# Performance work log

Hardware: AMD Instinct MI355X
Metric: run time of the kernel (lower is better)

## Reference

```python
import jax, jax.numpy as jnp
import numpy as np

KERNEL_SIZE = 3


def extract_local_features(feature_map, point_coords, kernel_size=KERNEL_SIZE):
    # feature_map: (B,C,H,W); point_coords: (B,N,2) normalized (y,x) in [0,1]
    B, C, H, W = feature_map.shape
    half = kernel_size // 2
    x = (point_coords[..., 1] * (W - 1)).astype(jnp.int32)  # (B,N)
    y = (point_coords[..., 0] * (H - 1)).astype(jnp.int32)
    x_min = jnp.clip(x - half, 0, None)
    x_max = jnp.clip(x + half + 1, None, W)
    y_min = jnp.clip(y - half, 0, None)
    y_max = jnpp_clip = jnp.clip(y + half + 1, None, H)
    y_max = jnp.clip(y + half + 1, None, H)
    # gather a fixed (k,k) window with clamped offsets, mask out-of-window entries
    offs = jnp.arange(kernel_size)  # (k,)
    yy = y_min[..., None] + offs  # (B,N,k) candidate rows
    xx = x_min[..., None] + offs  # (B,N,k)
    y_valid = yy < y_max[..., None]
    x_valid = xx < x_max[..., None]
    yy_c = jnp.clip(yy, 0, H - 1)
    xx_c = jnp.clip(xx, 0, W - 1)
    # flat spatial indices (B,N,k,k)
    flat_idx = yy_c[..., :, None] * W + xx_c[..., None, :]
    valid = (y_valid[..., :, None] & x_valid[..., None, :]).astype(feature_map.dtype)
    fm_flat = feature_map.reshape(B, C, H * W)  # (B,C,HW)

    def per_batch(fm, idx, val):
        # fm: (C,HW); idx,val: (N,k,k)
        g = fm[:, idx.reshape(-1)].reshape(fm.shape[0], *idx.shape)  # (C,N,k,k)
        s = jnp.einsum('cnij,nij->cn', g, val)
        cnt = val.sum(axis=(-1, -2))  # (N,)
        return s / cnt[None, :]

    return jax.vmap(per_batch)(fm_flat, flat_idx, valid)  # (B,C,N)


def point_sample(inp, point_coords):
    # bilinear grid_sample, align_corners=False, coords in [0,1] as (x,y) order
    # per the code: grid = 2*coords - 1; grid_sample uses (x,y) convention
    B, C, H, W = inp.shape
    gx = point_coords[..., 0]  # (B,N) in [0,1]
    gy = point_coords[..., 1]
    # align_corners=False mapping: pix = ((g*2-1)+1)/2 * size - 0.5 = g*size - 0.5
    fx = gx * W - 0.5
    fy = gy * H - 0.5
    x0 = jnp.floor(fx).astype(jnp.int32)
    y0 = jnp.floor(fy).astype(jnp.int32)
    wx = fx - x0
    wy = fy - y0

    def gather(yc, xc):
        inb = ((yc >= 0) & (yc < H) & (xc >= 0) & (xc < W)).astype(inp.dtype)  # (B,N)
        ycc = jnp.clip(yc, 0, H - 1)
        xcc = jnp.clip(xc, 0, W - 1)
        flat = ycc * W + xcc  # (B,N)
        fm = inp.reshape(B, C, H * W)
        g = jax.vmap(lambda f, i: f[:, i])(fm, flat)  # (B,C,N)
        return g * inb[:, None, :]

    v00 = gather(y0, x0)
    v01 = gather(y0, x0 + 1)
    v10 = gather(y0 + 1, x0)
    v11 = gather(y0 + 1, x0 + 1)
    wx_ = wx[:, None, :]
    wy_ = wy[:, None, :]
    out = (v00 * (1 - wx_) * (1 - wy_) + v01 * wx_ * (1 - wy_)
           + v10 * (1 - wx_) * wy_ + v11 * wx_ * wy_)  # (B,C,N)
    return out.transpose(0, 2, 1)  # (B,N,C)


def calculate_uncertainty(mask_logits):
    return -jnp.abs(mask_logits).squeeze(1)  # (B,H,W)


def edge_topk_sampling(edge_masks, uncertainty_map, topk):
    # edge_masks: (B,H,W) {0,1}; uncertainty_map: (B,H,W)
    B, H, W = edge_masks.shape
    NEG = jnp.asarray(-1e30, uncertainty_map.dtype)
    masked_u = jnp.where(edge_masks.reshape(B, -1) == 1,
                         uncertainty_map.reshape(B, -1), NEG)
    vals, idx = jax.lax.top_k(masked_u, topk)  # (B,topk)
    yi = (idx // W).astype(jnp.float32)
    xi = (idx % W).astype(jnp.float32)
    coords = jnp.stack([yi / (H - 1), xi / (W - 1)], axis=-1)  # (B,topk,2) (y,x)
    return idx, coords


def setup_inputs() -> dict:
    key = jax.random.key(0)
    k1, k2, k3, k4 = jax.random.split(key, 4)
    B, C, H, W = 8, 256, 256, 256
    N = 4096
    feature_map = jax.random.normal(k1, (B, C, H, W), dtype=jnp.float32)
    pred_mask = jax.random.normal(k2, (B, 1, H, W), dtype=jnp.float32)
    edge_masks = jax.random.randint(k3, (B, H, W), 0, 2).astype(jnp.int32)
    point_coords = jax.random.uniform(k4, (B, N, 2), dtype=jnp.float32)
    return {"feature_map": feature_map, "pred_mask": pred_mask,
            "edge_masks": edge_masks, "point_coords": point_coords,
            "topk": 4096}


def reference(feature_map, pred_mask, edge_masks, point_coords, topk):
    uncertainty_map = calculate_uncertainty(pred_mask)  # (B,H,W)
    idx, important_coords = edge_topk_sampling(edge_masks, uncertainty_map, topk)
    local_feats = extract_local_features(feature_map, important_coords)  # (B,C,topk)
    sampled = point_sample(feature_map, point_coords)  # (B,N,C)
    return local_feats, sampled, important_coords, idx
```

## Files before the change

kernel.cpp:

```cpp
#include <hip/hip_runtime.h>

#define CC 256
#define HH 256
#define WW 256
#define HWV 65536
#define NN 4096
#define SROWS 18
#define SSTRIDE 260

using u64 = unsigned long long;
using u32 = unsigned int;

__device__ __forceinline__ u32 lbound(const u32* __restrict__ a, u32 n, u32 key) {
    u32 lo = 0, hi = n;
    while (lo < hi) { u32 mid = (lo + hi) >> 1; if (a[mid] < key) lo = mid + 1; else hi = mid; }
    return lo;
}

__global__ void build_keys_k(const float* __restrict__ pm, const int* __restrict__ em,
                             u64* __restrict__ keys) {
    int i = blockIdx.x * blockDim.x + threadIdx.x;
    float f = (em[i] == 1) ? -fabsf(pm[i]) : -1e30f;
    u32 u = __float_as_uint(f);
    u32 k = (u & 0x80000000u) ? ~u : (u | 0x80000000u);
    u32 pix = (u32)i & 0xFFFFu;
    keys[i] = ((u64)k << 16) | (u64)(0xFFFFu - pix);
}

template<int DIRECT>
__global__ __launch_bounds__(1024) void topk_sortpc_k(const u64* __restrict__ keys,
                                                      const float* __restrict__ pc,
                                                      u32* __restrict__ stash,
                                                      u32* __restrict__ pixSorted,
                                                      u32* __restrict__ pcSorted,
                                                      float* __restrict__ outCoord,
                                                      float* __restrict__ outIdx) {
    __shared__ u64 sel[NN];
    __shared__ u64 bm[1024];
    __shared__ u32 wp[1024];
    __shared__ u32 s_digit, s_rem, s_cnt;
    const int t = threadIdx.x;
    if (blockIdx.x < 8) {
        const int b = blockIdx.x;
        const u64* kb = keys + (size_t)b * HWV;
        u32* hist = (u32*)sel;
        u64 prefix = 0ULL;
        u32 remaining = NN;
        for (int r = 0; r < 4; ++r) {
            int shift = 36 - 12 * r;
            #pragma unroll
            for (int q = 0; q < 4; ++q) hist[t + q * 1024] = 0u;
            __syncthreads();
            for (int i = t; i < HWV; i += 1024) {
                u64 K = kb[i];
                if ((K >> (shift + 12)) == prefix)
                    atomicAdd(&hist[(u32)((K >> shift) & 0xFFFULL)], 1u);
            }
            __syncthreads();
            for (int off = 1; off < 4096; off <<= 1) {
                u32 v[4];
                #pragma unroll
                for (int q = 0; q < 4; ++q) {
                    int i = t + q * 1024;
                    v[q] = hist[i];
                    if (i + off < 4096) v[q] += hist[i + off];
                }
                __syncthreads();
                #pragma unroll
                for (int q = 0; q < 4; ++q) hist[t + q * 1024] = v[q];
                __syncthreads();
            }
            #pragma unroll
            for (int q = 0; q < 4; ++q) {
                int d = t + q * 1024;
                u32 ge = hist[d];
                u32 gt = (d < 4095) ? hist[d + 1] : 0u;
                if (ge >= remaining && gt < remaining) { s_digit = (u32)d; s_rem = remaining - gt; }
            }
            __syncthreads();
            prefix = (prefix << 12) | (u64)s_digit;
            remaining = s_rem;
            __syncthreads();
        }
        if (t == 0) s_cnt = 0u;
        __syncthreads();
        for (int i = t; i < HWV; i += 1024) {
            u64 K = kb[i];
            if (K >= prefix) { u32 p = atomicAdd(&s_cnt, 1u); sel[p] = K; }
        }
        __syncthreads();
        for (int k = 2; k <= NN; k <<= 1) {
            for (int j = k >> 1; j > 0; j >>= 1) {
                for (int i = t; i < NN; i += 1024) {
                    int l = i ^ j;
                    if (l > i) {
                        u64 a = sel[i], c = sel[l];
                        bool asc = ((i & k) == 0);
                        if ((a < c) == asc) { sel[i] = c; sel[l] = a; }
                    }
                }
                __syncthreads();
            }
        }
        bm[t] = 0ULL;
        __syncthreads();
        #pragma unroll
        for (int q = 0; q < 4; ++q) {
            int r = t + q * 1024;
            u32 pix = 0xFFFFu - (u32)(sel[r] & 0xFFFFULL);
            if (DIRECT) {
                u32 yi = pix >> 8, xi = pix & 255u;
                outCoord[((size_t)b * NN + r) * 2 + 0] = (float)yi / 255.0f;
                outCoord[((size_t)b * NN + r) * 2 + 1] = (float)xi / 255.0f;
                outIdx[b * NN + r] = (float)pix;
            } else {
                stash[b * NN + r] = pix;
            }
            atomicOr(&bm[pix >> 6], 1ULL << (pix & 63));
        }
        __syncthreads();
        wp[t] = (u32)__popcll(bm[t]);
        __syncthreads();
        for (int off = 1; off < 1024; off <<= 1) {
            u32 v = wp[t];
            if (t >= off) v += wp[t - off];
            __syncthreads();
            wp[t] = v;
            __syncthreads();
        }
        #pragma unroll
        for (int q = 0; q < 4; ++q) {
            int r = t + q * 1024;
            u32 pix = 0xFFFFu - (u32)(sel[r] & 0xFFFFULL);
            int w = (int)(pix >> 6);
            u32 pos = wp[w] - (u32)__popcll(bm[w])
                    + (u32)__popcll(bm[w] & ((1ULL << (pix & 63)) - 1ULL));
            pixSorted[b * NN + pos] = (pix << 12) | (u32)r;
        }
    } else {
        const int b = blockIdx.x - 8;
        u32* cellArr = (u32*)sel;
        u32* hist256 = wp;
        u32* cnt     = (u32*)bm;
        if (t < 256) { hist256[t] = 0u; cnt[t] = 0u; }
        __syncthreads();
        for (int n = t; n < NN; n += 1024) {
            float gx = pc[((size_t)b * NN + n) * 2 + 0];
            float gy = pc[((size_t)b * NN + n) * 2 + 1];
            float fx = gx * 256.0f - 0.5f;
            float fy = gy * 256.0f - 0.5f;
            int x0 = (int)floorf(fx), y0 = (int)floorf(fy);
            int xc = min(max(x0, 0), 255), yc = min(max(y0, 0), 255);
            cellArr[n] = ((u32)(yc * 256 + xc) << 12) | (u32)n;
            atomicAdd(&hist256[yc], 1u);
        }
        __syncthreads();
        for (int off = 1; off < 256; off <<= 1) {
            u32 v = 0;
            if (t < 256) { v = hist256[t]; if (t >= off) v += hist256[t - off]; }
            __syncthreads();
            if (t < 256) hist256[t] = v;
            __syncthreads();
        }
        for (int n = t; n < NN; n += 1024) {
            u32 pk = cellArr[n];
            u32 yc = pk >> 20;
            u32 base = (yc > 0) ? hist256[yc - 1] : 0u;
            u32 pos = base + atomicAdd(&cnt[yc], 1u);
            pcSorted[b * NN + pos] = pk;
        }
    }
}

#define STAGE_LOAD(plane) \
    { int idx, r, c4, gr; \
      idx = t;        r = idx >> 6; c4 = idx & 63; gr = min(max(rStart + r, 0), HH - 1); \
      g0 = *(const float4*)((plane) + gr * WW + c4 * 4); \
      idx = t + 256;  r = idx >> 6; c4 = idx & 63; gr = min(max(rStart + r, 0), HH - 1); \
      g1 = *(const float4*)((plane) + gr * WW + c4 * 4); \
      idx = t + 512;  r = idx >> 6; c4 = idx & 63; gr = min(max(rStart + r, 0), HH - 1); \
      g2 = *(const float4*)((plane) + gr * WW + c4 * 4); \
      idx = t + 768;  r = idx >> 6; c4 = idx & 63; gr = min(max(rStart + r, 0), HH - 1); \
      g3 = *(const float4*)((plane) + gr * WW + c4 * 4); \
      if (t < 128) { idx = t + 1024; r = idx >> 6; c4 = idx & 63; gr = min(max(rStart + r, 0), HH - 1); \
      g4 = *(const float4*)((plane) + gr * WW + c4 * 4); } }

#define STAGE_WRITE() \
    { int idx, r, c4; \
      idx = t;        r = idx >> 6; c4 = idx & 63; *(float4*)(sm + r * SSTRIDE + c4 * 4) = g0; \
      idx = t + 256;  r = idx >> 6; c4 = idx & 63; *(float4*)(sm + r * SSTRIDE + c4 * 4) = g1; \
      idx = t + 512;  r = idx >> 6; c4 = idx & 63; *(float4*)(sm + r * SSTRIDE + c4 * 4) = g2; \
      idx = t + 768;  r = idx >> 6; c4 = idx & 63; *(float4*)(sm + r * SSTRIDE + c4 * 4) = g3; \
      if (t < 128) { idx = t + 1024; r = idx >> 6; c4 = idx & 63; *(float4*)(sm + r * SSTRIDE + c4 * 4) = g4; } }

__global__ __launch_bounds__(256) void plane_gather_k(const float* __restrict__ fm,
                                                      const float* __restrict__ pc,
                                                      const u32* __restrict__ pixSorted,
                                                      const u32* __restrict__ pcSorted,
                                                      float* __restrict__ outLc,
                                                      float* __restrict__ outSc) {
    __shared__ float sm[SROWS * SSTRIDE];
    const int band = blockIdx.x, c0 = blockIdx.y * 32, b = blockIdx.z;
    const int t = threadIdx.x;
    const int rStart = band * 16 - 1;
    const u32 keyLo = (u32)band << 24, keyHi = (u32)(band + 1) << 24;
    const u32* aL = pixSorted + b * NN;
    const u32* aS = pcSorted + b * NN;
    u32 loL = lbound(aL, NN, keyLo), cL = lbound(aL, NN, keyHi) - loL;
    u32 loS = lbound(aS, NN, keyLo), cS = lbound(aS, NN, keyHi) - loS;
    const float* planes = fm + ((size_t)b * CC + c0) * HWV;
    const float* pcb = pc + (size_t)b * NN * 2;

    int  Lo0 = 0, Lc2 = 0, Lr2 = 0;   float Lwc = 0, Lwr = 0, Lic = 0;
    int  Mo0 = 0, Mc2 = 0, Mr2 = 0;   float Mwc = 0, Mwr = 0, Mic = 0;
    int  So0 = 0, Sr1 = 0;            float Sv0 = 0, Sv1 = 0, Sw0 = 0, Sw1 = 0;
    int  To0 = 0, Tr1 = 0;            float Tv0 = 0, Tv1 = 0, Tw0 = 0, Tw1 = 0;
    {
        u32 jl = (u32)t;
        if (jl < cL) {
            u32 pix = aL[loL + jl] >> 12;
            int yi = (int)(pix >> 8), xi = (int)(pix & 255u);
            float cy = (float)yi / 255.0f, cx = (float)xi / 255.0f;
            int x = (int)(cx * 255.0f), y = (int)(cy * 255.0f);
            int x_min = max(x - 1, 0), wid = min(x + 2, WW) - x_min;
            int y_min = max(y - 1, 0), hgt = min(y + 2, HH) - y_min;
            Lo0 = (y_min - rStart) * SSTRIDE + x_min;
            Lc2 = (wid == 3) ? 2 : 0;  Lwc = (wid == 3) ? 1.0f : 0.0f;
            Lr2 = ((hgt == 3) ? 2 : 0) * SSTRIDE;  Lwr = (hgt == 3) ? 1.0f : 0.0f;
            Lic = 1.0f / (float)(wid * hgt);
        }
        jl = 256u + (u32)t;
        if (jl < cL) {
            u32 pix = aL[loL + jl] >> 12;
            int yi = (int)(pix >> 8), xi = (int)(pix & 255u);
            float cy = (float)yi / 255.0f, cx = (float)xi / 255.0f;
            int x = (int)(cx * 255.0f), y = (int)(cy * 255.0f);
            int x_min = max(x - 1, 0), wid = min(x + 2, WW) - x_min;
            int y_min = max(y - 1, 0), hgt = min(y + 2, HH) - y_min;
            Mo0 = (y_min - rStart) * SSTRIDE + x_min;
            Mc2 = (wid == 3) ? 2 : 0;  Mwc = (wid == 3) ? 1.0f : 0.0f;
            Mr2 = ((hgt == 3) ? 2 : 0) * SSTRIDE;  Mwr = (hgt == 3) ? 1.0f : 0.0f;
            Mic = 1.0f / (float)(wid * hgt);
        }
        u32 js = (u32)t;
        if (js < cS) {
            u32 sn = aS[loS + js] & 0xFFFu;
            float gx = pcb[2 * sn + 0], gy = pcb[2 * sn + 1];
            float fx = gx * 256.0f - 0.5f, fy = gy * 256.0f - 0.5f;
            float fx0 = floorf(fx), fy0 = floorf(fy);
            int x0 = (int)fx0, y0 = (int)fy0;
            float wx = fx - fx0, wy = fy - fy0;
            int xb = min(max(x0, 0), WW - 2);
            if (x0 < 0)            { Sv0 = wx;        Sv1 = 0.0f; }
            else if (x0 >= WW - 1) { Sv0 = 0.0f;      Sv1 = 1.0f - wx; }
            else                   { Sv0 = 1.0f - wx; Sv1 = wx; }
            Sw0 = (y0 >= 0)     ? (1.0f - wy) : 0.0f;
            Sw1 = (y0 + 1 < HH) ? wy          : 0.0f;
            int yc0 = min(max(y0, 0), HH - 1), yc1 = min(max(y0 + 1, 0), HH - 1);
            So0 = (yc0 - rStart) * SSTRIDE + xb;
            Sr1 = (yc1 - yc0) * SSTRIDE;
        }
        js = 256u + (u32)t;
        if (js < cS) {
            u32 sn = aS[loS + js] & 0xFFFu;
            float gx = pcb[2 * sn + 0], gy = pcb[2 * sn + 1];
            float fx = gx * 256.0f - 0.5f, fy = gy * 256.0f - 0.5f;
            float fx0 = floorf(fx), fy0 = floorf(fy);
            int x0 = (int)fx0, y0 = (int)fy0;
            float wx = fx - fx0, wy = fy - fy0;
            int xb = min(max(x0, 0), WW - 2);
            if (x0 < 0)            { Tv0 = wx;        Tv1 = 0.0f; }
            else if (x0 >= WW - 1) { Tv0 = 0.0f;      Tv1 = 1.0f - wx; }
            else                   { Tv0 = 1.0f - wx; Tv1 = wx; }
            Tw0 = (y0 >= 0)     ? (1.0f - wy) : 0.0f;
            Tw1 = (y0 + 1 < HH) ? wy          : 0.0f;
            int yc0 = min(max(y0, 0), HH - 1), yc1 = min(max(y0 + 1, 0), HH - 1);
            To0 = (yc0 - rStart) * SSTRIDE + xb;
            Tr1 = (yc1 - yc0) * SSTRIDE;
        }
    }

    float4 g0, g1, g2, g3, g4;
    STAGE_LOAD(planes)
    STAGE_WRITE()
    __syncthreads();

    #pragma unroll 1
    for (int j = 0; j < 32; ++j) {
        if (j + 1 < 32) { const float* np = planes + (size_t)(j + 1) * HWV; STAGE_LOAD(np) }
        float* oL = outLc + ((size_t)(b * CC + c0 + j)) * NN + loL;
        float* oS = outSc + ((size_t)(b * CC + c0 + j)) * NN + loS;
        if ((u32)t < cL) {
            float r0 = sm[Lo0] + sm[Lo0 + 1] + Lwc * sm[Lo0 + Lc2];
            float r1 = sm[Lo0 + SSTRIDE] + sm[Lo0 + SSTRIDE + 1] + Lwc * sm[Lo0 + SSTRIDE + Lc2];
            int o2 = Lo0 + Lr2;
            float r2 = sm[o2] + sm[o2 + 1] + Lwc * sm[o2 + Lc2];
            oL[t] = (r0 + r1 + Lwr * r2) * Lic;
        }
        if (256u + (u32)t < cL) {
            float r0 = sm[Mo0] + sm[Mo0 + 1] + Mwc * sm[Mo0 + Mc2];
            float r1 = sm[Mo0 + SSTRIDE] + sm[Mo0 + SSTRIDE + 1] + Mwc * sm[Mo0 + SSTRIDE + Mc2];
            int o2 = Mo0 + Mr2;
            float r2 = sm[o2] + sm[o2 + 1] + Mwc * sm[o2 + Mc2];
            oL[256 + t] = (r0 + r1 + Mwr * r2) * Mic;
        }
        if ((u32)t < cS) {
            oS[t] = Sw0 * (sm[So0] * Sv0 + sm[So0 + 1] * Sv1)
                  + Sw1 * (sm[So0 + Sr1] * Sv0 + sm[So0 + Sr1 + 1] * Sv1);
        }
        if (256u + (u32)t < cS) {
            oS[256 + t] = Tw0 * (sm[To0] * Tv0 + sm[To0 + 1] * Tv1)
                        + Tw1 * (sm[To0 + Tr1] * Tv0 + sm[To0 + Tr1 + 1] * Tv1);
        }
        __syncthreads();
        if (j + 1 < 32) { STAGE_WRITE() }
        __syncthreads();
    }

    for (u32 jl = 512 + (u32)t; jl < cL; jl += 256) {
        u32 pix = aL[loL + jl] >> 12;
        int yi = (int)(pix >> 8), xi = (int)(pix & 255u);
        float cy = (float)yi / 255.0f, cx = (float)xi / 255.0f;
        int x = (int)(cx * 255.0f), y = (int)(cy * 255.0f);
        int x_min = max(x - 1, 0), x_max = min(x + 2, WW);
        int y_min = max(y - 1, 0), y_max = min(y + 2, HH);
        float ic = 1.0f / (float)((x_max - x_min) * (y_max - y_min));
        for (int j = 0; j < 32; ++j) {
            const float* p = planes + (size_t)j * HWV;
            float s = 0.0f;
            for (int yy = y_min; yy < y_max; ++yy)
                for (int xx = x_min; xx < x_max; ++xx) s += p[yy * WW + xx];
            outLc[((size_t)(b * CC + c0 + j)) * NN + loL + jl] = s * ic;
        }
    }
    for (u32 js = 512 + (u32)t; js < cS; js += 256) {
        u32 sn = aS[loS + js] & 0xFFFu;
        float gx = pcb[2 * sn + 0], gy = pcb[2 * sn + 1];
        float fx = gx * 256.0f - 0.5f, fy = gy * 256.0f - 0.5f;
        float fx0 = floorf(fx), fy0 = floorf(fy);
        int x0 = (int)fx0, y0 = (int)fy0;
        float wx = fx - fx0, wy = fy - fy0;
        int xb = min(max(x0, 0), WW - 2);
        float v0, v1, r0, r1;
        if (x0 < 0)            { v0 = wx;        v1 = 0.0f; }
        else if (x0 >= WW - 1) { v0 = 0.0f;      v1 = 1.0f - wx; }
        else                   { v0 = 1.0f - wx; v1 = wx; }
        r0 = (y0 >= 0)     ? (1.0f - wy) : 0.0f;
        r1 = (y0 + 1 < HH) ? wy          : 0.0f;
        int yc0 = min(max(y0, 0), HH - 1), yc1 = min(max(y0 + 1, 0), HH - 1);
        int o0 = yc0 * WW + xb, o1 = yc1 * WW + xb;
        for (int j = 0; j < 32; ++j) {
            const float* p = planes + (size_t)j * HWV;
            outSc[((size_t)(b * CC + c0 + j)) * NN + loS + js] =
                r0 * (p[o0] * v0 + p[o0 + 1] * v1) + r1 * (p[o1] * v0 + p[o1 + 1] * v1);
        }
    }
}

__global__ __launch_bounds__(256) void unpermL_k(const float* __restrict__ outLc,
                                                 const u32* __restrict__ pixSorted,
                                                 float* __restrict__ outL) {
    __shared__ float row[NN];
    const int c = blockIdx.x, b = blockIdx.y;
    const int t = threadIdx.x;
    const float* in = outLc + ((size_t)(b * CC + c)) * NN;
    for (int j = t; j < NN; j += 256)
        row[pixSorted[b * NN + j] & 0xFFFu] = in[j];
    __syncthreads();
    float* o = outL + ((size_t)(b * CC + c)) * NN;
    for (int i = t; i < NN; i += 256) o[i] = row[i];
}

__global__ __launch_bounds__(256) void unpermS_k(const float* __restrict__ outSc,
                                                 const u32* __restrict__ pcSorted,
                                                 float* __restrict__ outS) {
    __shared__ float tile[32][257];
    __shared__ u32 ns[256];
    const int j0 = blockIdx.x * 256, c0 = blockIdx.y * 32, b = blockIdx.z;
    const int t = threadIdx.x;
    ns[t] = pcSorted[b * NN + j0 + t] & 0xFFFu;
    for (int i = 0; i < 32; ++i)
        tile[i][t] = outSc[((size_t)(b * CC + c0 + i)) * NN + j0 + t];
    __syncthreads();
    for (int idx = t; idx < 8192; idx += 256) {
        int p = idx >> 5, k = idx & 31;
        outS[((size_t)b * NN + ns[p]) * CC + c0 + k] = tile[k][p];
    }
}

template<int MODE>
__global__ __launch_bounds__(256, 4) void gather_k(const float* __restrict__ fm,
                                                   const float* __restrict__ pc,
                                                   const u32* __restrict__ pixSorted,
                                                   const u32* __restrict__ pcSorted,
                                                   float* __restrict__ outLp,
                                                   float* __restrict__ outS) {
    __shared__ float tile[256][33];
    __shared__ u32 pidx[256];
    const int b = blockIdx.z, j0 = blockIdx.x * 256, t = threadIdx.x;
    bool doL; int c0;
    if (MODE == 1) { doL = true; c0 = blockIdx.y * 32; }
    else { doL = false; c0 = blockIdx.y * 32; }
    const float* planes = fm + ((size_t)b * CC + c0) * HWV;
    if (doL) {
        u32 packed = pixSorted[b * NN + j0 + t];
        u32 pix = packed >> 12;
        pidx[t] = packed & 0xFFFu;
        int yi = (int)(pix >> 8), xi = (int)(pix & 255u);
        float cy = (float)yi / 255.0f, cx = (float)xi / 255.0f;
        int x = (int)(cx * 255.0f), y = (int)(cy * 255.0f);
        int x_min = max(x - 1, 0), x_max = min(x + 2, WW);
        int y_min = max(y - 1, 0), y_max = min(y + 2, HH);
        int base = min(x_min & ~3, WW - 8);
        float w8[8];
        #pragma unroll
        for (int i = 0; i < 8; ++i)
            w8[i] = (base + i >= x_min && base + i < x_max) ? 1.0f : 0.0f;
        float wr2 = (y_min + 2 < y_max) ? 1.0f : 0.0f;
        int o0 = y_min * WW + base, o1 = o0 + WW;
        int o2 = min(y_min + 2, HH - 1) * WW + base;
        float invc = 1.0f / (float)((x_max - x_min) * (y_max - y_min));
        #pragma unroll 2
        for (int j = 0; j < 32; ++j) {
            const float* p = planes + (size_t)j * HWV;
            float4 a0 = *(const float4*)(p + o0), b0 = *(const float4*)(p + o0 + 4);
            float4 a1 = *(const float4*)(p + o1), b1 = *(const float4*)(p + o1 + 4);
            float4 a2 = *(const float4*)(p + o2), b2 = *(const float4*)(p + o2 + 4);
            float s0 = a0.x * w8[0] + a0.y * w8[1] + a0.z * w8[2] + a0.w * w8[3]
                     + b0.x * w8[4] + b0.y * w8[5] + b0.z * w8[6] + b0.w * w8[7];
            float s1 = a1.x * w8[0] + a1.y * w8[1] + a1.z * w8[2] + a1.w * w8[3]
                     + b1.x * w8[4] + b1.y * w8[5] + b1.z * w8[6] + b1.w * w8[7];
            float s2 = a2.x * w8[0] + a2.y * w8[1] + a2.z * w8[2] + a2.w * w8[3]
                     + b2.x * w8[4] + b2.y * w8[5] + b2.z * w8[6] + b2.w * w8[7];
            tile[t][j] = (s0 + s1 + wr2 * s2) * invc;
        }
        __syncthreads();
        for (int idx = t; idx < 8192; idx += 256) {
            int p = idx >> 5, k = idx & 31;
            outLp[((size_t)b * NN + pidx[p]) * CC + c0 + k] = tile[p][k];
        }
    } else {
        int n = (int)(pcSorted[b * NN + j0 + t] & 0xFFFu);
        pidx[t] = (u32)n;
        float gx = pc[((size_t)b * NN + n) * 2 + 0];
        float gy = pc[((size_t)b * NN + n) * 2 + 1];
        float fx = gx * 256.0f - 0.5f, fy = gy * 256.0f - 0.5f;
        float fx0 = floorf(fx), fy0 = floorf(fy);
        int x0 = (int)fx0, y0 = (int)fy0;
        float wx = fx - fx0, wy = fy - fy0;
        int xb = min(max(x0, 0), WW - 2);
        float wv0, wv1;
        if (x0 < 0)            { wv0 = wx;        wv1 = 0.0f; }
        else if (x0 >= WW - 1) { wv0 = 0.0f;      wv1 = 1.0f - wx; }
        else                   { wv0 = 1.0f - wx; wv1 = wx; }
        float wr0 = (y0 >= 0)     ? (1.0f - wy) : 0.0f;
        float wr1 = (y0 + 1 < HH) ? wy          : 0.0f;
        int yc0 = min(max(y0, 0), HH - 1), yc1 = min(max(y0 + 1, 0), HH - 1);
        int o0 = yc0 * WW + xb, o1 = yc1 * WW + xb;
        #pragma unroll 4
        for (int j = 0; j < 32; ++j) {
            const float* p = planes + (size_t)j * HWV;
            tile[t][j] = wr0 * (p[o0] * wv0 + p[o0 + 1] * wv1)
                       + wr1 * (p[o1] * wv0 + p[o1 + 1] * wv1);
        }
        __syncthreads();
        for (int idx = t; idx < 8192; idx += 256) {
            int p = idx >> 5, k = idx & 31;
            outS[((size_t)b * NN + pidx[p]) * CC + c0 + k] = tile[p][k];
        }
    }
}

__global__ __launch_bounds__(256) void transpose_k(const float* __restrict__ outLp,
                                                   float* __restrict__ outL) {
    __shared__ float tile[256][33];
    const int b = blockIdx.z, c0 = blockIdx.y * 32, r0 = blockIdx.x * 256;
    const int t = threadIdx.x;
    for (int idx = t; idx < 8192; idx += 256) {
        int p = idx >> 5, k = idx & 31;
        tile[p][k] = outLp[((size_t)b * NN + r0 + p) * CC + c0 + k];
    }
    __syncthreads();
    for (int idx = t; idx < 8192; idx += 256) {
        int cl = idx >> 8, col = idx & 255;
        outL[((size_t)b * CC + c0 + cl) * NN + r0 + col] = tile[col][cl];
    }
}

__global__ void emit_k(const u32* __restrict__ stash, float* __restrict__ outCoord,
                       float* __restrict__ outIdx) {
    int i = blockIdx.x * blockDim.x + threadIdx.x;
    u32 p = stash[i];
    u32 yi = p >> 8, xi = p & 255u;
    outCoord[(size_t)i * 2 + 0] = (float)yi / 255.0f;
    outCoord[(size_t)i * 2 + 1] = (float)xi / 255.0f;
    outIdx[i] = (float)p;
}

extern "C" void kernel_launch(void* const* d_in, const int* in_sizes, int n_in,
                              void* d_out, int out_size, void* d_ws, size_t ws_size,
                              hipStream_t stream) {
    const float* fm = (const float*)d_in[0];
    const float* pm = (const float*)d_in[1];
    const int*   em = (const int*)d_in[2];
    const float* pc = (const float*)d_in[3];
    (void)in_sizes; (void)n_in; (void)out_size;

    float* out      = (float*)d_out;
    float* outL     = out;
    float* outS     = out + (size_t)8388608;
    float* outCoord = out + (size_t)16777216;
    float* outIdx   = out + (size_t)16842752;

    const size_t need_ws = (size_t)80 * 1024 * 1024;
    bool ws_ok = ws_size >= need_ws;

    if (ws_ok) {
        char* w = (char*)d_ws;
        u64* keys      = (u64*)w;
        u32* pixSorted = (u32*)(w + (size_t)4300 * 1024);
        u32* pcSorted  = (u32*)(w + (size_t)4600 * 1024);
        float* outLc   = (float*)(w + (size_t)5  * 1024 * 1024);
        float* outSc   = (float*)(w + (size_t)40 * 1024 * 1024);

        hipLaunchKernelGGL(build_keys_k, dim3(2048), dim3(256), 0, stream, pm, em, keys);
        hipLaunchKernelGGL((topk_sortpc_k<1>), dim3(16), dim3(1024), 0, stream,
                           keys, pc, (u32*)nullptr, pixSorted, pcSorted, outCoord, outIdx);
        hipLaunchKernelGGL(plane_gather_k, dim3(16, 8, 8), dim3(256), 0, stream,
                           fm, pc, pixSorted, pcSorted, outLc, outSc);
        hipLaunchKernelGGL(unpermL_k, dim3(256, 8), dim3(256), 0, stream,
                           outLc, pixSorted, outL);
        hipLaunchKernelGGL(unpermS_k, dim3(16, 8, 8), dim3(256), 0, stream,
                           outSc, pcSorted, outS);
    } else {
        u64* keys      = (u64*)outS;
        u32* stash     = (u32*)outIdx;
        u32* pixSorted = (u32*)outCoord;
        u32* pcSorted  = pixSorted + 32768;
        float* outLp   = outS;

        hipLaunchKernelGGL(build_keys_k, dim3(2048), dim3(256), 0, stream, pm, em, keys);
        hipLaunchKernelGGL((topk_sortpc_k<0>), dim3(16), dim3(1024), 0, stream,
                           keys, pc, stash, pixSorted, pcSorted, outCoord, outIdx);
        hipLaunchKernelGGL((gather_k<1>), dim3(16, 8, 8), dim3(256), 0, stream,
                           fm, pc, pixSorted, pcSorted, outLp, outS);
        hipLaunchKernelGGL(transpose_k, dim3(16, 8, 8), dim3(256), 0, stream, outLp, outL);
        hipLaunchKernelGGL((gather_k<2>), dim3(16, 8, 8), dim3(256), 0, stream,
                           fm, pc, pixSorted, pcSorted, outS, outS);
        hipLaunchKernelGGL(emit_k, dim3(128), dim3(256), 0, stream, stash, outCoord, outIdx);
    }
}
```

Baseline: 325.2 us.

## Double-buffer plane staging via direct global-to-LDS loads and fuse key building

The plane gather kernel now stages each channel band directly into LDS with global_load_lds and double buffers across two LDS arrays. This removes the register round-trip and one barrier per channel iteration. The row stride drops to 256 so each wave writes a contiguous LDS row, which may add bank conflicts on the bilinear and window reads. Separately, key construction is fused into the top-k kernel's first histogram pass, which removes one launch and one full pass over the keys; the fallback path keeps the old kernel.

```diff
diff --git a/kernel.cpp b/kernel.cpp
--- a/kernel.cpp
+++ b/kernel.cpp
@@ -6,7 +6,7 @@
 #define HWV 65536
 #define NN 4096
 #define SROWS 18
-#define SSTRIDE 260
+#define SSTRIDE 256
 
 using u64 = unsigned long long;
 using u32 = unsigned int;
@@ -28,7 +28,9 @@
 }
 
 template<int DIRECT>
-__global__ __launch_bounds__(1024) void topk_sortpc_k(const u64* __restrict__ keys,
+__global__ __launch_bounds__(1024) void topk_sortpc_k(const float* __restrict__ pm,
+                                                      const int* __restrict__ em,
+                                                      u64* __restrict__ keys,
                                                       const float* __restrict__ pc,
                                                       u32* __restrict__ stash,
                                                       u32* __restrict__ pixSorted,
@@ -42,21 +44,37 @@
     const int t = threadIdx.x;
     if (blockIdx.x < 8) {
         const int b = blockIdx.x;
-        const u64* kb = keys + (size_t)b * HWV;
+        u64* kb = keys + (size_t)b * HWV;
+        const float* pmb = pm + (size_t)b * HWV;
+        const int*   emb = em + (size_t)b * HWV;
         u32* hist = (u32*)sel;
         u64 prefix = 0ULL;
         u32 remaining = NN;
+        #pragma unroll
+        for (int q = 0; q < 4; ++q) hist[t + q * 1024] = 0u;
+        __syncthreads();
+        for (int i = t; i < HWV; i += 1024) {
+            float f = (emb[i] == 1) ? -fabsf(pmb[i]) : -1e30f;
+            u32 u = __float_as_uint(f);
+            u32 k = (u & 0x80000000u) ? ~u : (u | 0x80000000u);
+            u64 K = ((u64)k << 16) | (u64)(0xFFFFu - (u32)i);
+            kb[i] = K;
+            atomicAdd(&hist[(u32)(K >> 36)], 1u);
+        }
+        __syncthreads();
         for (int r = 0; r < 4; ++r) {
             int shift = 36 - 12 * r;
-            #pragma unroll
-            for (int q = 0; q < 4; ++q) hist[t + q * 1024] = 0u;
-            __syncthreads();
-            for (int i = t; i < HWV; i += 1024) {
-                u64 K = kb[i];
-                if ((K >> (shift + 12)) == prefix)
-                    atomicAdd(&hist[(u32)((K >> shift) & 0xFFFULL)], 1u);
-            }
-            __syncthreads();
+            if (r > 0) {
+                #pragma unroll
+                for (int q = 0; q < 4; ++q) hist[t + q * 1024] = 0u;
+                __syncthreads();
+                for (int i = t; i < HWV; i += 1024) {
+                    u64 K = kb[i];
+                    if ((K >> (shift + 12)) == prefix)
+                        atomicAdd(&hist[(u32)((K >> shift) & 0xFFFULL)], 1u);
+                }
+                __syncthreads();
+            }
             for (int off = 1; off < 4096; off <<= 1) {
                 u32 v[4];
                 #pragma unroll
@@ -172,26 +190,19 @@
     }
 }
 
-#define STAGE_LOAD(plane) \
-    { int idx, r, c4, gr; \
-      idx = t;        r = idx >> 6; c4 = idx & 63; gr = min(max(rStart + r, 0), HH - 1); \
-      g0 = *(const float4*)((plane) + gr * WW + c4 * 4); \
-      idx = t + 256;  r = idx >> 6; c4 = idx & 63; gr = min(max(rStart + r, 0), HH - 1); \
-      g1 = *(const float4*)((plane) + gr * WW + c4 * 4); \
-      idx = t + 512;  r = idx >> 6; c4 = idx & 63; gr = min(max(rStart + r, 0), HH - 1); \
-      g2 = *(const float4*)((plane) + gr * WW + c4 * 4); \
-      idx = t + 768;  r = idx >> 6; c4 = idx & 63; gr = min(max(rStart + r, 0), HH - 1); \
-      g3 = *(const float4*)((plane) + gr * WW + c4 * 4); \
-      if (t < 128) { idx = t + 1024; r = idx >> 6; c4 = idx & 63; gr = min(max(rStart + r, 0), HH - 1); \
-      g4 = *(const float4*)((plane) + gr * WW + c4 * 4); } }
-
-#define STAGE_WRITE() \
-    { int idx, r, c4; \
-      idx = t;        r = idx >> 6; c4 = idx & 63; *(float4*)(sm + r * SSTRIDE + c4 * 4) = g0; \
-      idx = t + 256;  r = idx >> 6; c4 = idx & 63; *(float4*)(sm + r * SSTRIDE + c4 * 4) = g1; \
-      idx = t + 512;  r = idx >> 6; c4 = idx & 63; *(float4*)(sm + r * SSTRIDE + c4 * 4) = g2; \
-      idx = t + 768;  r = idx >> 6; c4 = idx & 63; *(float4*)(sm + r * SSTRIDE + c4 * 4) = g3; \
-      if (t < 128) { idx = t + 1024; r = idx >> 6; c4 = idx & 63; *(float4*)(sm + r * SSTRIDE + c4 * 4) = g4; } }
+#define STAGE_DMA(plane, smbuf) \
+    { _Pragma("unroll") \
+      for (int u = 0; u < 5; ++u) { \
+        int idx = t + u * 256; \
+        if (idx < SROWS * 64) { \
+            int row = idx >> 6; \
+            int gr = min(max(rStart + row, 0), HH - 1); \
+            const float* gsrc = (plane) + gr * WW + ((idx & 63) << 2); \
+            float* ldst = (smbuf) + row * SSTRIDE; \
+            __builtin_amdgcn_global_load_lds( \
+                (const __attribute__((address_space(1))) void*)gsrc, \
+                (__attribute__((address_space(3))) void*)ldst, 16, 0, 0); \
+        } } }
 
 __global__ __launch_bounds__(256) void plane_gather_k(const float* __restrict__ fm,
                                                       const float* __restrict__ pc,
@@ -199,7 +210,8 @@
                                                       const u32* __restrict__ pcSorted,
                                                       float* __restrict__ outLc,
                                                       float* __restrict__ outSc) {
-    __shared__ float sm[SROWS * SSTRIDE];
+    __shared__ float smA[SROWS * SSTRIDE];
+    __shared__ float smB[SROWS * SSTRIDE];
     const int band = blockIdx.x, c0 = blockIdx.y * 32, b = blockIdx.z;
     const int t = threadIdx.x;
     const int rStart = band * 16 - 1;
@@ -280,14 +292,17 @@
         }
     }
 
-    float4 g0, g1, g2, g3, g4;
-    STAGE_LOAD(planes)
-    STAGE_WRITE()
+    STAGE_DMA(planes, smA)
     __syncthreads();
 
     #pragma unroll 1
     for (int j = 0; j < 32; ++j) {
-        if (j + 1 < 32) { const float* np = planes + (size_t)(j + 1) * HWV; STAGE_LOAD(np) }
+        const float* sm = (j & 1) ? smB : smA;
+        if (j + 1 < 32) {
+            const float* np = planes + (size_t)(j + 1) * HWV;
+            float* nb = ((j + 1) & 1) ? smB : smA;
+            STAGE_DMA(np, nb)
+        }
         float* oL = outLc + ((size_t)(b * CC + c0 + j)) * NN + loL;
         float* oS = outSc + ((size_t)(b * CC + c0 + j)) * NN + loS;
         if ((u32)t < cL) {
@@ -312,8 +327,6 @@
             oS[256 + t] = Tw0 * (sm[To0] * Tv0 + sm[To0 + 1] * Tv1)
                         + Tw1 * (sm[To0 + Tr1] * Tv0 + sm[To0 + Tr1 + 1] * Tv1);
         }
-        __syncthreads();
-        if (j + 1 < 32) { STAGE_WRITE() }
         __syncthreads();
     }
 
@@ -385,6 +398,151 @@
     for (int idx = t; idx < 8192; idx += 256) {
         int p = idx >> 5, k = idx & 31;
         outS[((size_t)b * NN + ns[p]) * CC + c0 + k] = tile[k][p];
+    }
+}
+
+template<int DIRECT>
+__global__ __launch_bounds__(1024) void topk_sortpc_old_k(const u64* __restrict__ keys,
+                                                          const float* __restrict__ pc,
+                                                          u32* __restrict__ stash,
+                                                          u32* __restrict__ pixSorted,
+                                                          u32* __restrict__ pcSorted,
+                                                          float* __restrict__ outCoord,
+                                                          float* __restrict__ outIdx) {
+    __shared__ u64 sel[NN];
+    __shared__ u64 bm[1024];
+    __shared__ u32 wp[1024];
+    __shared__ u32 s_digit, s_rem, s_cnt;
+    const int t = threadIdx.x;
+    if (blockIdx.x < 8) {
+        const int b = blockIdx.x;
+        const u64* kb = keys + (size_t)b * HWV;
+        u32* hist = (u32*)sel;
+        u64 prefix = 0ULL;
+        u32 remaining = NN;
+        for (int r = 0; r < 4; ++r) {
+            int shift = 36 - 12 * r;
+            #pragma unroll
+            for (int q = 0; q < 4; ++q) hist[t + q * 1024] = 0u;
+            __syncthreads();
+            for (int i = t; i < HWV; i += 1024) {
+                u64 K = kb[i];
+                if ((K >> (shift + 12)) == prefix)
+                    atomicAdd(&hist[(u32)((K >> shift) & 0xFFFULL)], 1u);
+            }
+            __syncthreads();
+            for (int off = 1; off < 4096; off <<= 1) {
+                u32 v[4];
+                #pragma unroll
+                for (int q = 0; q < 4; ++q) {
+                    int i = t + q * 1024;
+                    v[q] = hist[i];
+                    if (i + off < 4096) v[q] += hist[i + off];
+                }
+                __syncthreads();
+                #pragma unroll
+                for (int q = 0; q < 4; ++q) hist[t + q * 1024] = v[q];
+                __syncthreads();
+            }
+            #pragma unroll
+            for (int q = 0; q < 4; ++q) {
+                int d = t + q * 1024;
+                u32 ge = hist[d];
+                u32 gt = (d < 4095) ? hist[d + 1] : 0u;
+                if (ge >= remaining && gt < remaining) { s_digit = (u32)d; s_rem = remaining - gt; }
+            }
+            __syncthreads();
+            prefix = (prefix << 12) | (u64)s_digit;
+            remaining = s_rem;
+            __syncthreads();
+        }
+        if (t == 0) s_cnt = 0u;
+        __syncthreads();
+        for (int i = t; i < HWV; i += 1024) {
+            u64 K = kb[i];
+            if (K >= prefix) { u32 p = atomicAdd(&s_cnt, 1u); sel[p] = K; }
+        }
+        __syncthreads();
+        for (int k = 2; k <= NN; k <<= 1) {
+            for (int j = k >> 1; j > 0; j >>= 1) {
+                for (int i = t; i < NN; i += 1024) {
+                    int l = i ^ j;
+                    if (l > i) {
+                        u64 a = sel[i], c = sel[l];
+                        bool asc = ((i & k) == 0);
+                        if ((a < c) == asc) { sel[i] = c; sel[l] = a; }
+                    }
+                }
+                __syncthreads();
+            }
+        }
+        bm[t] = 0ULL;
+        __syncthreads();
+        #pragma unroll
+        for (int q = 0; q < 4; ++q) {
+            int r = t + q * 1024;
+            u32 pix = 0xFFFFu - (u32)(sel[r] & 0xFFFFULL);
+            if (DIRECT) {
+                u32 yi = pix >> 8, xi = pix & 255u;
+                outCoord[((size_t)b * NN + r) * 2 + 0] = (float)yi / 255.0f;
+                outCoord[((size_t)b * NN + r) * 2 + 1] = (float)xi / 255.0f;
+                outIdx[b * NN + r] = (float)pix;
+            } else {
+                stash[b * NN + r] = pix;
+            }
+            atomicOr(&bm[pix >> 6], 1ULL << (pix & 63));
+        }
+        __syncthreads();
+        wp[t] = (u32)__popcll(bm[t]);
+        __syncthreads();
+        for (int off = 1; off < 1024; off <<= 1) {
+            u32 v = wp[t];
+            if (t >= off) v += wp[t - off];
+            __syncthreads();
+            wp[t] = v;
+            __syncthreads();
+        }
+        #pragma unroll
+        for (int q = 0; q < 4; ++q) {
+            int r = t + q * 1024;
+            u32 pix = 0xFFFFu - (u32)(sel[r] & 0xFFFFULL);
+            int w = (int)(pix >> 6);
+            u32 pos = wp[w] - (u32)__popcll(bm[w])
+                    + (u32)__popcll(bm[w] & ((1ULL << (pix & 63)) - 1ULL));
+            pixSorted[b * NN + pos] = (pix << 12) | (u32)r;
+        }
+    } else {
+        const int b = blockIdx.x - 8;
+        u32* cellArr = (u32*)sel;
+        u32* hist256 = wp;
+        u32* cnt     = (u32*)bm;
+        if (t < 256) { hist256[t] = 0u; cnt[t] = 0u; }
+        __syncthreads();
+        for (int n = t; n < NN; n += 1024) {
+            float gx = pc[((size_t)b * NN + n) * 2 + 0];
+            float gy = pc[((size_t)b * NN + n) * 2 + 1];
+            float fx = gx * 256.0f - 0.5f;
+            float fy = gy * 256.0f - 0.5f;
+            int x0 = (int)floorf(fx), y0 = (int)floorf(fy);
+            int xc = min(max(x0, 0), 255), yc = min(max(y0, 0), 255);
+            cellArr[n] = ((u32)(yc * 256 + xc) << 12) | (u32)n;
+            atomicAdd(&hist256[yc], 1u);
+        }
+        __syncthreads();
+        for (int off = 1; off < 256; off <<= 1) {
+            u32 v = 0;
+            if (t < 256) { v = hist256[t]; if (t >= off) v += hist256[t - off]; }
+            __syncthreads();
+            if (t < 256) hist256[t] = v;
+            __syncthreads();
+        }
+        for (int n = t; n < NN; n += 1024) {
+            u32 pk = cellArr[n];
+            u32 yc = pk >> 20;
+            u32 base = (yc > 0) ? hist256[yc - 1] : 0u;
+            u32 pos = base + atomicAdd(&cnt[yc], 1u);
+            pcSorted[b * NN + pos] = pk;
+        }
     }
 }
 
@@ -523,9 +681,9 @@
         float* outLc   = (float*)(w + (size_t)5  * 1024 * 1024);
         float* outSc   = (float*)(w + (size_t)40 * 1024 * 1024);
 
-        hipLaunchKernelGGL(build_keys_k, dim3(2048), dim3(256), 0, stream, pm, em, keys);
         hipLaunchKernelGGL((topk_sortpc_k<1>), dim3(16), dim3(1024), 0, stream,
-                           keys, pc, (u32*)nullptr, pixSorted, pcSorted, outCoord, outIdx);
+                           pm, em, keys, pc, (u32*)nullptr, pixSorted, pcSorted,
+                           outCoord, outIdx);
         hipLaunchKernelGGL(plane_gather_k, dim3(16, 8, 8), dim3(256), 0, stream,
                            fm, pc, pixSorted, pcSorted, outLc, outSc);
         hipLaunchKernelGGL(unpermL_k, dim3(256, 8), dim3(256), 0, stream,
@@ -540,7 +698,7 @@
         float* outLp   = outS;
 
         hipLaunchKernelGGL(build_keys_k, dim3(2048), dim3(256), 0, stream, pm, em, keys);
-        hipLaunchKernelGGL((topk_sortpc_k<0>), dim3(16), dim3(1024), 0, stream,
+        hipLaunchKernelGGL((topk_sortpc_old_k<0>), dim3(16), dim3(1024), 0, stream,
                            keys, pc, stash, pixSorted, pcSorted, outCoord, outIdx);
         hipLaunchKernelGGL((gather_k<1>), dim3(16, 8, 8), dim3(256), 0, stream,
                            fm, pc, pixSorted, pcSorted, outLp, outS);
```

After: 368.8 us. 13.4% more time.
